# Kernel optimization log

Measured on AMD Instinct MI355X. Metric: run time of the kernel, lower is better.

The kernel has to match this reference:

```python
import jax, jax.numpy as jnp
import numpy as np

H = 1152; NH = 16; HD = 72; INTER = 4304; DEPTH = 4
C = 3; T = 2; P = 16; G = 48; M = 2; S = G * G
MERGED = H * M * M; OUT = 2048; ROT = HD // 2  # rotary_pos_emb_dim = head_dim//2


def _ln(x, w, b, eps=1e-6):
    # manual LayerNorm decomposition (mean/var/rsqrt), fp32 like the original
    m = x.mean(-1, keepdims=True)
    xc = x - m
    v = (xc * xc).mean(-1, keepdims=True)
    return w * (xc * jax.lax.rsqrt(v + eps)) + b


def _gelu(x):
    return jax.nn.gelu(x, approximate=True)  # tanh approximation


def _rot_half(x):
    h = x.shape[-1] // 2
    return jnp.concatenate([-x[..., h:], x[..., :h]], axis=-1)


def _pos_ids():
    # Qwen merge-pattern token order: 2x2 spatial blocks are contiguous
    ids = np.arange(G * G).reshape(G // M, M, G // M, M).transpose(0, 2, 1, 3).reshape(-1)
    return jnp.asarray(ids, dtype=jnp.int32)


def setup_inputs() -> dict:
    key = jax.random.key(0)
    ks = jax.random.split(key, 16)
    w = lambda k, shape: jax.random.normal(k, shape, jnp.float32) * 0.02
    return {
        'pixel_values': jax.random.normal(ks[0], (S, C * T * P * P), jnp.float32),
        'cu_seqlens': jnp.array([0, S], jnp.int32),
        'conv_w': w(ks[1], (H, C, T, P, P)),
        'conv_b': jnp.zeros((H,), jnp.float32),
        'pos_tab': w(ks[2], (G * G, H)),
        'ln1_w': jnp.ones((DEPTH, H), jnp.float32), 'ln1_b': jnp.zeros((DEPTH, H), jnp.float32),
        'ln2_w': jnp.ones((DEPTH, H), jnp.float32), 'ln2_b': jnp.zeros((DEPTH, H), jnp.float32),
        'qkv_w': w(ks[3], (DEPTH, 3 * H, H)), 'qkv_b': jnp.zeros((DEPTH, 3 * H), jnp.float32),
        'proj_w': w(ks[4], (DEPTH, H, H)), 'proj_b': jnp.zeros((DEPTH, H), jnp.float32),
        'fc1_w': w(ks[5], (DEPTH, INTER, H)), 'fc1_b': jnp.zeros((DEPTH, INTER), jnp.float32),
        'fc2_w': w(ks[6], (DEPTH, H, INTER)), 'fc2_b': jnp.zeros((DEPTH, H), jnp.float32),
        'm_norm_w': jnp.ones((H,), jnp.float32), 'm_norm_b': jnp.zeros((H,), jnp.float32),
        'm_fc1_w': w(ks[7], (MERGED, MERGED)), 'm_fc1_b': jnp.zeros((MERGED,), jnp.float32),
        'm_fc2_w': w(ks[8], (OUT, MERGED)), 'm_fc2_b': jnp.zeros((OUT,), jnp.float32),
    }


def reference(pixel_values, cu_seqlens, conv_w, conv_b, pos_tab,
              ln1_w, ln1_b, ln2_w, ln2_b, qkv_w, qkv_b, proj_w, proj_b,
              fc1_w, fc1_b, fc2_w, fc2_b, m_norm_w, m_norm_b,
              m_fc1_w, m_fc1_b, m_fc2_w, m_fc2_b):
    pos_ids = _pos_ids()
    # Conv3d with stride == kernel over pre-extracted patches == matmul
    x = pixel_values @ conv_w.reshape(H, -1).T + conv_b            # [S, H]
    x = x + pos_tab[pos_ids]
    # 2D rotary: h-freqs and w-freqs each ROT/2 dims, concat -> ROT, dup -> HD
    inv_freq = 1.0 / (10000.0 ** (jnp.arange(0, ROT, 2, dtype=jnp.float32) / ROT))
    hp = (pos_ids // G).astype(jnp.float32)
    wp = (pos_ids % G).astype(jnp.float32)
    freqs = jnp.concatenate([hp[:, None] * inv_freq, wp[:, None] * inv_freq], axis=-1)  # [S, ROT]
    emb = jnp.concatenate([freqs, freqs], axis=-1)                 # [S, HD]
    cos = jnp.cos(emb)[:, None, :]                                 # [S, 1, HD]
    sin = jnp.sin(emb)[:, None, :]
    # varlen attention: block-diagonal mask from cu_seqlens
    seg = jnp.searchsorted(cu_seqlens, jnp.arange(S), side='right')
    mask = jnp.where(seg[:, None] == seg[None, :], 0.0, -1e9).astype(jnp.float32)
    scale = 1.0 / np.sqrt(HD)
    for i in range(DEPTH):
        h = _ln(x, ln1_w[i], ln1_b[i])
        qkv = (h @ qkv_w[i].T + qkv_b[i]).reshape(S, 3, NH, HD)
        q, k, v = qkv[:, 0], qkv[:, 1], qkv[:, 2]
        q = q * cos + _rot_half(q) * sin
        k = k * cos + _rot_half(k) * sin
        scores = jnp.einsum('qhd,khd->hqk', q, k) * scale + mask
        attn = jax.nn.softmax(scores, axis=-1)
        o = jnp.einsum('hqk,khd->qhd', attn, v).reshape(S, H)
        x = x + o @ proj_w[i].T + proj_b[i]
        h2 = _ln(x, ln2_w[i], ln2_b[i])
        x = x + _gelu(h2 @ fc1_w[i].T + fc1_b[i]) @ fc2_w[i].T + fc2_b[i]
    # patch merger: pre-merge LN -> reshape to merged -> fc1 -> gelu(tanh) -> fc2
    y = _ln(x, m_norm_w, m_norm_b).reshape(-1, MERGED)             # [S/4, MERGED]
    return _gelu(y @ m_fc1_w.T + m_fc1_b) @ m_fc2_w.T + m_fc2_b   # [S/4, OUT]
```

## Files before the change

### kernel.cpp

```cpp
#include <hip/hip_runtime.h>
#include <hip/hip_bf16.h>
#include <math.h>

#define S 2304
#define HDIM 1152
#define NHEAD 16
#define HD 72
#define INTER 4304
#define INTERP 4352
#define DEPTH 4
#define MERGED 4608
#define OUTD 2048
#define KIN 1536
#define NSPLIT 2
#define KHALF (S / NSPLIT)

typedef float f4 __attribute__((ext_vector_type(4)));
typedef short s8v __attribute__((ext_vector_type(8)));

__device__ __forceinline__ int pos_id_of(int s) {
  int a = s / 96;
  int r = s % 96;
  int b = r >> 2;
  int c = (r >> 1) & 1;
  int d = r & 1;
  return a * 96 + c * 48 + b * 2 + d;
}

__device__ __forceinline__ float gelu_f(float v) {
  const float c = 0.7978845608028654f;
  float t = tanhf(c * (v + 0.044715f * v * v * v));
  return 0.5f * v * (1.f + t);
}

__device__ __forceinline__ unsigned short f2b(float f) {
  unsigned int u = __float_as_uint(f);
  u += 0x7fffu + ((u >> 16) & 1u);
  return (unsigned short)(u >> 16);
}
__device__ __forceinline__ float b2f(unsigned short u) {
  return __uint_as_float(((unsigned int)u) << 16);
}

__device__ __forceinline__ void gload16(const void* g, void* l) {
  __builtin_amdgcn_global_load_lds(
      (const __attribute__((address_space(1))) void*)g,
      (__attribute__((address_space(3))) void*)l, 16, 0, 0);
}

__device__ __forceinline__ int xcd_swz(int flat, int nwg) {
  int q = nwg >> 3, r8 = nwg & 7;
  int xcd = flat & 7, lin = flat >> 3;
  return (xcd < r8 ? xcd * (q + 1) : r8 * (q + 1) + (xcd - r8) * q) + lin;
}

__global__ void __launch_bounds__(256) cvt_kernel(
    const float* __restrict__ src, unsigned short* __restrict__ dst,
    int N, int Ksrc, int Kdst)
{
  int idx = blockIdx.x * 256 + threadIdx.x;
  int kc = Kdst >> 3;
  if (idx >= N * kc) return;
  int r = idx / kc;
  int c8 = (idx % kc) << 3;
  const float* sp = src + (size_t)r * Ksrc + c8;
  unsigned short outv[8];
#pragma unroll
  for (int e = 0; e < 8; ++e)
    outv[e] = (c8 + e < Ksrc) ? f2b(sp[e]) : (unsigned short)0;
  *(uint4*)(dst + (size_t)r * Kdst + c8) = *(uint4*)outv;
}

__global__ void __launch_bounds__(256) gemm_bf16_kernel(
    const unsigned short* __restrict__ A, const unsigned short* __restrict__ B,
    const float* __restrict__ bias, const float* __restrict__ resid,
    void* __restrict__ Cout, int M, int Nreal, int K,
    int lda, int ldb, int ldc, int act, int outbf)
{
  __shared__ unsigned short Asm[2][128 * 32];
  __shared__ unsigned short Bsm[2][128 * 32];
  const int tid = threadIdx.x;
  const int lane = tid & 63;
  const int wv = tid >> 6;
  const int wr = wv >> 1, wc = wv & 1;

  int flat = blockIdx.y * gridDim.x + blockIdx.x;
  int swz = xcd_swz(flat, gridDim.x * gridDim.y);
  const int bm = (swz / gridDim.x) * 128;
  const int bn = (swz % gridDim.x) * 128;

  const int g8 = (lane >> 4) << 3;
  const int lr = lane & 15;

  const int srow = wv * 32 + (lane >> 2);
  const int kcol = (lane & 3) << 3;
  int ar0 = bm + srow;      if (ar0 >= M) ar0 = M - 1;
  int ar1 = bm + srow + 16; if (ar1 >= M) ar1 = M - 1;
  int br0 = bn + srow;      if (br0 >= Nreal) br0 = Nreal - 1;
  int br1 = bn + srow + 16; if (br1 >= Nreal) br1 = Nreal - 1;
  const unsigned short* Ag0 = A + (size_t)ar0 * lda + kcol;
  const unsigned short* Ag1 = A + (size_t)ar1 * lda + kcol;
  const unsigned short* Bg0 = B + (size_t)br0 * ldb + kcol;
  const unsigned short* Bg1 = B + (size_t)br1 * ldb + kcol;

  f4 acc[4][4];
#pragma unroll
  for (int m = 0; m < 4; ++m)
#pragma unroll
    for (int n = 0; n < 4; ++n) { acc[m][n].x = 0.f; acc[m][n].y = 0.f; acc[m][n].z = 0.f; acc[m][n].w = 0.f; }

  const int nt = K >> 5;
  gload16(Ag0, &Asm[0][(wv * 32) * 32]);
  gload16(Ag1, &Asm[0][(wv * 32 + 16) * 32]);
  gload16(Bg0, &Bsm[0][(wv * 32) * 32]);
  gload16(Bg1, &Bsm[0][(wv * 32 + 16) * 32]);
  asm volatile("s_waitcnt vmcnt(0)" ::: "memory");
  __syncthreads();

  int cur = 0;
  for (int t = 0; t < nt; ++t) {
    if (t + 1 < nt) {
      int ko = (t + 1) << 5;
      gload16(Ag0 + ko, &Asm[cur ^ 1][(wv * 32) * 32]);
      gload16(Ag1 + ko, &Asm[cur ^ 1][(wv * 32 + 16) * 32]);
      gload16(Bg0 + ko, &Bsm[cur ^ 1][(wv * 32) * 32]);
      gload16(Bg1 + ko, &Bsm[cur ^ 1][(wv * 32 + 16) * 32]);
    }
    s8v af[4], bf[4];
#pragma unroll
    for (int m = 0; m < 4; ++m)
      af[m] = *(const s8v*)&Asm[cur][(wr * 64 + m * 16 + lr) * 32 + g8];
#pragma unroll
    for (int n = 0; n < 4; ++n)
      bf[n] = *(const s8v*)&Bsm[cur][(wc * 64 + n * 16 + lr) * 32 + g8];
#pragma unroll
    for (int m = 0; m < 4; ++m)
#pragma unroll
      for (int n = 0; n < 4; ++n)
        acc[m][n] = __builtin_amdgcn_mfma_f32_16x16x32_bf16(af[m], bf[n], acc[m][n], 0, 0, 0);
    asm volatile("s_waitcnt vmcnt(0)" ::: "memory");
    __syncthreads();
    cur ^= 1;
  }

  const int g4 = (lane >> 4) << 2;
#pragma unroll
  for (int m = 0; m < 4; ++m) {
    int r = bm + wr * 64 + m * 16 + g4;
#pragma unroll
    for (int n = 0; n < 4; ++n) {
      int cidx = bn + wc * 64 + n * 16 + lr;
      float bb = (cidx < Nreal) ? bias[cidx] : 0.f;
#pragma unroll
      for (int j = 0; j < 4; ++j) {
        int rr = r + j;
        if (rr < M) {
          float v = acc[m][n][j] + bb;
          if (act) v = gelu_f(v);
          if (cidx >= Nreal) v = 0.f;
          if (resid) v += resid[(size_t)rr * ldc + cidx];
          if (outbf) ((unsigned short*)Cout)[(size_t)rr * ldc + cidx] = f2b(v);
          else       ((float*)Cout)[(size_t)rr * ldc + cidx] = v;
        }
      }
    }
  }
}

__global__ void __launch_bounds__(256) gemm_bf16_splitk_kernel(
    const unsigned short* __restrict__ A, const unsigned short* __restrict__ B,
    float* __restrict__ Cpart, int M, int N, int Kc, int lda, int ldb)
{
  __shared__ unsigned short Asm[2][128 * 32];
  __shared__ unsigned short Bsm[2][128 * 32];
  const int tid = threadIdx.x;
  const int lane = tid & 63;
  const int wv = tid >> 6;
  const int wr = wv >> 1, wc = wv & 1;

  int flat = blockIdx.y * gridDim.x + blockIdx.x;
  int swz = xcd_swz(flat, gridDim.x * gridDim.y);
  const int bm = (swz / gridDim.x) * 128;
  const int bn = (swz % gridDim.x) * 128;
  const int z = blockIdx.z;
  const int kbase = z * Kc;

  const int g8 = (lane >> 4) << 3;
  const int lr = lane & 15;

  const int srow = wv * 32 + (lane >> 2);
  const int kcol = (lane & 3) << 3;
  int ar0 = bm + srow;      if (ar0 >= M) ar0 = M - 1;
  int ar1 = bm + srow + 16; if (ar1 >= M) ar1 = M - 1;
  int br0 = bn + srow;      if (br0 >= N) br0 = N - 1;
  int br1 = bn + srow + 16; if (br1 >= N) br1 = N - 1;
  const unsigned short* Ag0 = A + (size_t)ar0 * lda + kbase + kcol;
  const unsigned short* Ag1 = A + (size_t)ar1 * lda + kbase + kcol;
  const unsigned short* Bg0 = B + (size_t)br0 * ldb + kbase + kcol;
  const unsigned short* Bg1 = B + (size_t)br1 * ldb + kbase + kcol;

  f4 acc[4][4];
#pragma unroll
  for (int m = 0; m < 4; ++m)
#pragma unroll
    for (int n = 0; n < 4; ++n) { acc[m][n].x = 0.f; acc[m][n].y = 0.f; acc[m][n].z = 0.f; acc[m][n].w = 0.f; }

  const int nt = Kc >> 5;
  gload16(Ag0, &Asm[0][(wv * 32) * 32]);
  gload16(Ag1, &Asm[0][(wv * 32 + 16) * 32]);
  gload16(Bg0, &Bsm[0][(wv * 32) * 32]);
  gload16(Bg1, &Bsm[0][(wv * 32 + 16) * 32]);
  asm volatile("s_waitcnt vmcnt(0)" ::: "memory");
  __syncthreads();

  int cur = 0;
  for (int t = 0; t < nt; ++t) {
    if (t + 1 < nt) {
      int ko = (t + 1) << 5;
      gload16(Ag0 + ko, &Asm[cur ^ 1][(wv * 32) * 32]);
      gload16(Ag1 + ko, &Asm[cur ^ 1][(wv * 32 + 16) * 32]);
      gload16(Bg0 + ko, &Bsm[cur ^ 1][(wv * 32) * 32]);
      gload16(Bg1 + ko, &Bsm[cur ^ 1][(wv * 32 + 16) * 32]);
    }
    s8v af[4], bf[4];
#pragma unroll
    for (int m = 0; m < 4; ++m)
      af[m] = *(const s8v*)&Asm[cur][(wr * 64 + m * 16 + lr) * 32 + g8];
#pragma unroll
    for (int n = 0; n < 4; ++n)
      bf[n] = *(const s8v*)&Bsm[cur][(wc * 64 + n * 16 + lr) * 32 + g8];
#pragma unroll
    for (int m = 0; m < 4; ++m)
#pragma unroll
      for (int n = 0; n < 4; ++n)
        acc[m][n] = __builtin_amdgcn_mfma_f32_16x16x32_bf16(af[m], bf[n], acc[m][n], 0, 0, 0);
    asm volatile("s_waitcnt vmcnt(0)" ::: "memory");
    __syncthreads();
    cur ^= 1;
  }

  float* Cz = Cpart + (size_t)z * M * N;
  const int g4 = (lane >> 4) << 2;
#pragma unroll
  for (int m = 0; m < 4; ++m) {
    int r = bm + wr * 64 + m * 16 + g4;
#pragma unroll
    for (int n = 0; n < 4; ++n) {
      int cidx = bn + wc * 64 + n * 16 + lr;
      if (cidx < N) {
#pragma unroll
        for (int j = 0; j < 4; ++j) {
          int rr = r + j;
          if (rr < M) Cz[(size_t)rr * N + cidx] = acc[m][n][j];
        }
      }
    }
  }
}

__global__ void __launch_bounds__(256) combine_gemm_kernel(
    const float* __restrict__ Cpart, int nz, const float* __restrict__ bias,
    const float* __restrict__ resid, float* __restrict__ out, int M, int N)
{
  int idx = blockIdx.x * 256 + threadIdx.x;
  int total = (M * N) >> 2;
  if (idx >= total) return;
  int r = idx / (N >> 2);
  int c4 = (idx % (N >> 2)) << 2;
  size_t off = (size_t)r * N + c4;
  float4 s = *(const float4*)(Cpart + off);
  for (int z = 1; z < nz; ++z) {
    float4 p = *(const float4*)(Cpart + (size_t)z * M * N + off);
    s.x += p.x; s.y += p.y; s.z += p.z; s.w += p.w;
  }
  float4 b = *(const float4*)(bias + c4);
  s.x += b.x; s.y += b.y; s.z += b.z; s.w += b.w;
  if (resid) {
    float4 rv = *(const float4*)(resid + off);
    s.x += rv.x; s.y += rv.y; s.z += rv.z; s.w += rv.w;
  }
  *(float4*)(out + off) = s;
}

__global__ void __launch_bounds__(256) ln_kernel(const float* __restrict__ xin,
    const float* __restrict__ w, const float* __restrict__ b, unsigned short* __restrict__ out)
{
  __shared__ float red[8];
  const int row = blockIdx.x;
  const float* xr = xin + (size_t)row * HDIM;
  float s = 0.f;
  for (int i = threadIdx.x; i < HDIM; i += 256) s += xr[i];
#pragma unroll
  for (int off = 32; off > 0; off >>= 1) s += __shfl_down(s, off);
  if ((threadIdx.x & 63) == 0) red[threadIdx.x >> 6] = s;
  __syncthreads();
  float mean = (red[0] + red[1] + red[2] + red[3]) * (1.f / HDIM);
  float s2 = 0.f;
  for (int i = threadIdx.x; i < HDIM; i += 256) { float d = xr[i] - mean; s2 += d * d; }
#pragma unroll
  for (int off = 32; off > 0; off >>= 1) s2 += __shfl_down(s2, off);
  __syncthreads();
  if ((threadIdx.x & 63) == 0) red[threadIdx.x >> 6] = s2;
  __syncthreads();
  float var = (red[0] + red[1] + red[2] + red[3]) * (1.f / HDIM);
  float rstd = rsqrtf(var + 1e-6f);
  for (int i = threadIdx.x; i < HDIM; i += 256)
    out[(size_t)row * HDIM + i] = f2b(w[i] * ((xr[i] - mean) * rstd) + b[i]);
}

__global__ void __launch_bounds__(256) add_pos_kernel(float* __restrict__ x, const float* __restrict__ pos_tab)
{
  int s = blockIdx.x;
  int pid = pos_id_of(s);
  const float* pr = pos_tab + (size_t)pid * HDIM;
  float* xr = x + (size_t)s * HDIM;
  for (int i = threadIdx.x; i < HDIM; i += 256) xr[i] += pr[i];
}

__global__ void rope_tables_kernel(float* __restrict__ cosT, float* __restrict__ sinT)
{
  int s = blockIdx.x;
  int j = threadIdx.x;
  if (j >= 36) return;
  int pid = pos_id_of(s);
  float hp = (float)(pid / 48);
  float wp = (float)(pid % 48);
  int f = (j < 18) ? j : (j - 18);
  float inv = powf(10000.f, -(2.f * (float)f) / 36.f);
  float ang = ((j < 18) ? hp : wp) * inv;
  cosT[s * 36 + j] = cosf(ang);
  sinT[s * 36 + j] = sinf(ang);
}

__global__ void seg_kernel(const int* __restrict__ cu, int n_cu, int* __restrict__ seg)
{
  int i = blockIdx.x * 256 + threadIdx.x;
  if (i >= S) return;
  int s = 0;
  for (int t = 0; t < n_cu; ++t) s += (cu[t] <= i) ? 1 : 0;
  seg[i] = s;
}

__global__ void __launch_bounds__(256) rope_kernel(unsigned short* __restrict__ qkv,
    const float* __restrict__ cosT, const float* __restrict__ sinT)
{
  int idx = blockIdx.x * 256 + threadIdx.x;
  int d = idx % 36; int t = idx / 36;
  int hh = t % NHEAD; t /= NHEAD;
  int qk = t & 1; int s = t >> 1;
  unsigned short* base = qkv + (size_t)s * 3456 + qk * 1152 + hh * 72;
  float c = cosT[s * 36 + d], sn = sinT[s * 36 + d];
  float x0 = b2f(base[d]), x1 = b2f(base[d + 36]);
  base[d] = f2b(x0 * c - x1 * sn);
  base[d + 36] = f2b(x1 * c + x0 * sn);
}

#define KT 64
#define KSL 88
#define ASCALE 0.11785113019775793f

__global__ void __launch_bounds__(256) flash_mfma_kernel(
    const unsigned short* __restrict__ qkv, unsigned short* __restrict__ opart,
    float* __restrict__ ml, const int* __restrict__ seg)
{
  __shared__ __align__(16) unsigned short Ks[64 * KSL];
  __shared__ __align__(16) unsigned short Vt[80 * 72];
  __shared__ __align__(16) unsigned short Ps[4][16 * 72];

  const int tid = threadIdx.x;
  const int lane = tid & 63;
  const int wv = tid >> 6;
  const int g = lane >> 4;
  const int c = lane & 15;

  int flat = (blockIdx.z * NHEAD + blockIdx.y) * (S / 64) + blockIdx.x;
  int swz = xcd_swz(flat, (S / 64) * NHEAD * NSPLIT);
  const int q0 = (swz % (S / 64)) * 64;
  const int hh = (swz / (S / 64)) % NHEAD;
  const int sidx = swz / ((S / 64) * NHEAD);
  const int kbeg = sidx * KHALF;

  for (int i = tid; i < 64 * 8; i += 256) {
    int r = i >> 3, cc = i & 7;
    *(unsigned int*)&Ks[r * KSL + 72 + cc * 2] = 0u;
  }
  for (int i = tid; i < 288; i += 256)
    *(unsigned int*)&Vt[72 * 72 + i * 2] = 0u;

  s8v qf[3];
  {
    const int qrow = q0 + wv * 16 + c;
    const unsigned short* qb = qkv + (size_t)qrow * 3456 + hh * HD;
#pragma unroll
    for (int ks = 0; ks < 3; ++ks) {
      int k = ks * 32 + g * 8;
      if (k <= 64) qf[ks] = *(const s8v*)(qb + k);
      else {
        s8v z;
#pragma unroll
        for (int t = 0; t < 8; ++t) z[t] = 0;
        qf[ks] = z;
      }
    }
  }

  int msg[4];
#pragma unroll
  for (int j = 0; j < 4; ++j) msg[j] = seg[q0 + wv * 16 + g * 4 + j];

  float mj[4], lj[4];
#pragma unroll
  for (int j = 0; j < 4; ++j) { mj[j] = -1e30f; lj[j] = 0.f; }
  f4 acco[5];
#pragma unroll
  for (int n = 0; n < 5; ++n) { acco[n].x = 0.f; acco[n].y = 0.f; acco[n].z = 0.f; acco[n].w = 0.f; }

  uint4 kreg[3], vreg[3];

#define STAGE_LOAD(KT0)                                                                  \
  {                                                                                      \
    _Pragma("unroll")                                                                    \
    for (int ii = 0; ii < 3; ++ii) {                                                     \
      int idx = tid + ii * 256;                                                          \
      if (idx < 576) {                                                                   \
        int rK = idx / 9, cK = idx % 9;                                                  \
        kreg[ii] = *(const uint4*)(qkv + (size_t)((KT0) + rK) * 3456 + 1152 + hh * HD + cK * 8); \
        int rV = idx & 63, cV = idx >> 6;                                                \
        vreg[ii] = *(const uint4*)(qkv + (size_t)((KT0) + rV) * 3456 + 2304 + hh * HD + cV * 8); \
      }                                                                                  \
    }                                                                                    \
  }

#define STAGE_WRITE()                                                                    \
  {                                                                                      \
    _Pragma("unroll")                                                                    \
    for (int ii = 0; ii < 3; ++ii) {                                                     \
      int idx = tid + ii * 256;                                                          \
      if (idx < 576) {                                                                   \
        int rK = idx / 9, cK = idx % 9;                                                  \
        *(uint4*)&Ks[rK * KSL + cK * 8] = kreg[ii];                                      \
        int rV = idx & 63, cV = idx >> 6;                                                \
        unsigned short vv[8];                                                            \
        *(uint4*)vv = vreg[ii];                                                          \
        _Pragma("unroll")                                                                \
        for (int e = 0; e < 8; ++e) Vt[(cV * 8 + e) * 72 + rV] = vv[e];                  \
      }                                                                                  \
    }                                                                                    \
  }

  STAGE_LOAD(kbeg);
  asm volatile("s_waitcnt vmcnt(0)" ::: "memory");
  STAGE_WRITE();
  asm volatile("s_waitcnt lgkmcnt(0)" ::: "memory");
  __builtin_amdgcn_s_barrier();
  __builtin_amdgcn_sched_barrier(0);

  for (int k0 = kbeg; k0 < kbeg + KHALF; k0 += KT) {
    const bool more = (k0 + KT < kbeg + KHALF);
    if (more) STAGE_LOAD(k0 + KT);

    int sgn[4];
#pragma unroll
    for (int n = 0; n < 4; ++n) sgn[n] = seg[k0 + n * 16 + c];

    f4 accs[4];
#pragma unroll
    for (int n = 0; n < 4; ++n) { accs[n].x = 0.f; accs[n].y = 0.f; accs[n].z = 0.f; accs[n].w = 0.f; }
#pragma unroll
    for (int ks = 0; ks < 3; ++ks) {
      const int koff = (ks < 2) ? (ks * 32 + g * 8) : 64;
#pragma unroll
      for (int n = 0; n < 4; ++n) {
        s8v bk = *(const s8v*)&Ks[(n * 16 + c) * KSL + koff];
        accs[n] = __builtin_amdgcn_mfma_f32_16x16x32_bf16(qf[ks], bk, accs[n], 0, 0, 0);
      }
    }

    float sc[4][4], mx[4];
#pragma unroll
    for (int j = 0; j < 4; ++j) mx[j] = -1e30f;
#pragma unroll
    for (int n = 0; n < 4; ++n)
#pragma unroll
      for (int j = 0; j < 4; ++j) {
        float v = accs[n][j] * ASCALE + ((sgn[n] == msg[j]) ? 0.f : -1e9f);
        sc[n][j] = v;
        mx[j] = fmaxf(mx[j], v);
      }
#pragma unroll
    for (int j = 0; j < 4; ++j) {
      mx[j] = fmaxf(mx[j], __shfl_xor(mx[j], 1));
      mx[j] = fmaxf(mx[j], __shfl_xor(mx[j], 2));
      mx[j] = fmaxf(mx[j], __shfl_xor(mx[j], 4));
      mx[j] = fmaxf(mx[j], __shfl_xor(mx[j], 8));
    }
    float alpha[4], rs[4];
#pragma unroll
    for (int j = 0; j < 4; ++j) {
      float mn = fmaxf(mj[j], mx[j]);
      alpha[j] = __expf(mj[j] - mn);
      mj[j] = mn;
      rs[j] = 0.f;
    }
    float pv[4][4];
#pragma unroll
    for (int n = 0; n < 4; ++n)
#pragma unroll
      for (int j = 0; j < 4; ++j) {
        float p = __expf(sc[n][j] - mj[j]);
        pv[n][j] = p;
        rs[j] += p;
      }
#pragma unroll
    for (int j = 0; j < 4; ++j) {
      rs[j] += __shfl_xor(rs[j], 1);
      rs[j] += __shfl_xor(rs[j], 2);
      rs[j] += __shfl_xor(rs[j], 4);
      rs[j] += __shfl_xor(rs[j], 8);
      lj[j] = lj[j] * alpha[j] + rs[j];
    }
#pragma unroll
    for (int n = 0; n < 4; ++n)
#pragma unroll
      for (int j = 0; j < 4; ++j)
        Ps[wv][(g * 4 + j) * 72 + n * 16 + c] = f2b(pv[n][j]);

#pragma unroll
    for (int n = 0; n < 5; ++n)
#pragma unroll
      for (int j = 0; j < 4; ++j) acco[n][j] *= alpha[j];

    asm volatile("s_waitcnt lgkmcnt(0)" ::: "memory");
    __builtin_amdgcn_sched_barrier(0);

#pragma unroll
    for (int ks = 0; ks < 2; ++ks) {
      s8v pa = *(const s8v*)&Ps[wv][c * 72 + ks * 32 + g * 8];
#pragma unroll
      for (int n = 0; n < 5; ++n) {
        s8v vb = *(const s8v*)&Vt[(n * 16 + c) * 72 + ks * 32 + g * 8];
        acco[n] = __builtin_amdgcn_mfma_f32_16x16x32_bf16(pa, vb, acco[n], 0, 0, 0);
      }
    }

    asm volatile("s_waitcnt lgkmcnt(0)" ::: "memory");
    __builtin_amdgcn_s_barrier();
    if (more) {
      asm volatile("s_waitcnt vmcnt(0)" ::: "memory");
      STAGE_WRITE();
      asm volatile("s_waitcnt lgkmcnt(0)" ::: "memory");
    }
    __builtin_amdgcn_s_barrier();
    __builtin_amdgcn_sched_barrier(0);
  }

  unsigned short* op = opart + (size_t)(sidx * NHEAD + hh) * S * 72;
#pragma unroll
  for (int n = 0; n < 5; ++n) {
    int col = n * 16 + c;
    if (col < HD) {
#pragma unroll
      for (int j = 0; j < 4; ++j) {
        int row = q0 + wv * 16 + g * 4 + j;
        op[(size_t)row * 72 + col] = f2b(acco[n][j]);
      }
    }
  }
  if (c == 0) {
#pragma unroll
    for (int j = 0; j < 4; ++j) {
      int row = q0 + wv * 16 + g * 4 + j;
      float2 v; v.x = mj[j]; v.y = lj[j];
      *(float2*)&ml[((size_t)(sidx * NHEAD + hh) * S + row) * 2] = v;
    }
  }
}

__global__ void __launch_bounds__(256) attn_combine_kernel(
    const unsigned short* __restrict__ opart, const float* __restrict__ ml,
    unsigned short* __restrict__ oout)
{
  int idx = blockIdx.x * 256 + threadIdx.x;
  int d = idx % 72;
  int row = (idx / 72) % S;
  int hh = idx / (72 * S);
  size_t b1 = (size_t)hh * S + row;
  size_t b2 = (size_t)(NHEAD + hh) * S + row;
  float m1 = ml[b1 * 2], l1 = ml[b1 * 2 + 1];
  float m2 = ml[b2 * 2], l2 = ml[b2 * 2 + 1];
  float ms = fmaxf(m1, m2);
  float a1 = __expf(m1 - ms), a2 = __expf(m2 - ms);
  float l = a1 * l1 + a2 * l2;
  float o = (a1 * b2f(opart[b1 * 72 + d]) + a2 * b2f(opart[b2 * 72 + d])) / l;
  oout[(size_t)row * HDIM + hh * 72 + d] = f2b(o);
}

extern "C" void kernel_launch(void* const* d_in, const int* in_sizes, int n_in,
                              void* d_out, int out_size, void* d_ws, size_t ws_size,
                              hipStream_t stream)
{
  (void)n_in; (void)out_size; (void)ws_size;
  const float* pix    = (const float*)d_in[0];
  const int*   cu     = (const int*)d_in[1];
  const int    n_cu   = in_sizes[1];
  const float* conv_w = (const float*)d_in[2];
  const float* conv_b = (const float*)d_in[3];
  const float* pos_tab= (const float*)d_in[4];
  const float* ln1_w  = (const float*)d_in[5];
  const float* ln1_b  = (const float*)d_in[6];
  const float* ln2_w  = (const float*)d_in[7];
  const float* ln2_b  = (const float*)d_in[8];
  const float* qkv_w  = (const float*)d_in[9];
  const float* qkv_b  = (const float*)d_in[10];
  const float* proj_w = (const float*)d_in[11];
  const float* proj_b = (const float*)d_in[12];
  const float* fc1_w  = (const float*)d_in[13];
  const float* fc1_b  = (const float*)d_in[14];
  const float* fc2_w  = (const float*)d_in[15];
  const float* fc2_b  = (const float*)d_in[16];
  const float* mn_w   = (const float*)d_in[17];
  const float* mn_b   = (const float*)d_in[18];
  const float* mf1_w  = (const float*)d_in[19];
  const float* mf1_b  = (const float*)d_in[20];
  const float* mf2_w  = (const float*)d_in[21];
  const float* mf2_b  = (const float*)d_in[22];
  float* out = (float*)d_out;

  float*    x      = (float*)d_ws;
  unsigned short* h_bf   = (unsigned short*)(x + (size_t)S * HDIM);
  unsigned short* qkv_bf = h_bf + (size_t)S * HDIM;
  unsigned short* A_bf   = qkv_bf + (size_t)S * 3456;
  unsigned short* Wbuf   = A_bf + (size_t)S * INTERP;
  float*    cosT   = (float*)(Wbuf + (size_t)MERGED * MERGED);
  float*    sinT   = cosT + (size_t)S * 36;
  int*      seg    = (int*)(sinT + (size_t)S * 36);
  unsigned short* pix_bf = A_bf;
  unsigned short* opart  = A_bf;
  float*    ml     = (float*)(A_bf + (size_t)NSPLIT * NHEAD * S * 72);
  float*    part_h = (float*)h_bf;
  float*    part_q = (float*)qkv_bf;

  auto cvt = [&](const float* src, unsigned short* dst, int N, int Ksrc, int Kdst) {
    int total = N * (Kdst >> 3);
    cvt_kernel<<<(total + 255) / 256, 256, 0, stream>>>(src, dst, N, Ksrc, Kdst);
  };
  auto gemm = [&](const unsigned short* A, const unsigned short* B, const float* bias,
                  const float* resid, void* C, int M, int N, int K,
                  int lda, int ldb, int ldc, int act, int outbf) {
    gemm_bf16_kernel<<<dim3((N + 127) / 128, (M + 127) / 128), 256, 0, stream>>>(
        A, B, bias, resid, C, M, N, K, lda, ldb, ldc, act, outbf);
  };
  auto gemm_sk = [&](const unsigned short* A, const unsigned short* B, float* part,
                     const float* bias, const float* resid, float* C,
                     int M, int N, int K, int nz, int lda, int ldb) {
    gemm_bf16_splitk_kernel<<<dim3(N / 128, (M + 127) / 128, nz), 256, 0, stream>>>(
        A, B, part, M, N, K / nz, lda, ldb);
    combine_gemm_kernel<<<((M * N / 4) + 255) / 256, 256, 0, stream>>>(
        part, nz, bias, resid, C, M, N);
  };

  cvt(pix, pix_bf, S, KIN, KIN);
  cvt(conv_w, Wbuf, HDIM, KIN, KIN);
  gemm_sk(pix_bf, Wbuf, part_h, conv_b, nullptr, x, S, HDIM, KIN, 2, KIN, KIN);
  add_pos_kernel<<<S, 256, 0, stream>>>(x, pos_tab);
  rope_tables_kernel<<<S, 64, 0, stream>>>(cosT, sinT);
  seg_kernel<<<(S + 255) / 256, 256, 0, stream>>>(cu, n_cu, seg);

  for (int layer = 0; layer < DEPTH; ++layer) {
    ln_kernel<<<S, 256, 0, stream>>>(x, ln1_w + layer * HDIM, ln1_b + layer * HDIM, h_bf);
    cvt(qkv_w + (size_t)layer * 3456 * HDIM, Wbuf, 3456, HDIM, HDIM);
    gemm(h_bf, Wbuf, qkv_b + layer * 3456, nullptr, qkv_bf, S, 3456, HDIM, HDIM, HDIM, 3456, 0, 1);
    rope_kernel<<<(S * 2 * NHEAD * 36) / 256, 256, 0, stream>>>(qkv_bf, cosT, sinT);
    flash_mfma_kernel<<<dim3(S / 64, NHEAD, NSPLIT), 256, 0, stream>>>(qkv_bf, opart, ml, seg);
    attn_combine_kernel<<<(NHEAD * S * 72) / 256, 256, 0, stream>>>(opart, ml, h_bf);
    cvt(proj_w + (size_t)layer * HDIM * HDIM, Wbuf, HDIM, HDIM, HDIM);
    gemm_sk(h_bf, Wbuf, part_q, proj_b + layer * HDIM, x, x, S, HDIM, HDIM, 3, HDIM, HDIM);
    ln_kernel<<<S, 256, 0, stream>>>(x, ln2_w + layer * HDIM, ln2_b + layer * HDIM, h_bf);
    cvt(fc1_w + (size_t)layer * INTER * HDIM, Wbuf, INTER, HDIM, HDIM);
    gemm(h_bf, Wbuf, fc1_b + layer * INTER, nullptr, A_bf, S, INTER, HDIM, HDIM, HDIM, INTERP, 1, 1);
    cvt(fc2_w + (size_t)layer * HDIM * INTER, Wbuf, HDIM, INTER, INTERP);
    gemm_sk(A_bf, Wbuf, part_h, fc2_b + layer * HDIM, x, x, S, HDIM, INTERP, 2, INTERP, INTERP);
  }

  ln_kernel<<<S, 256, 0, stream>>>(x, mn_w, mn_b, h_bf);
  cvt(mf1_w, Wbuf, MERGED, MERGED, MERGED);
  gemm(h_bf, Wbuf, mf1_b, nullptr, A_bf, 576, MERGED, MERGED, MERGED, MERGED, MERGED, 1, 1);
  cvt(mf2_w, Wbuf, OUTD, MERGED, MERGED);
  gemm_sk(A_bf, Wbuf, part_h, mf2_b, nullptr, out, 576, OUTD, MERGED, 4, MERGED, MERGED);
}
```

Before: 1.879 ms.

## Add 64-row GEMM tile kernel and restructure flash attention softmax layout

Adds a new GEMM kernel with 64x128 tiles, used for the QKV, fc1 and merger fc1 projections, so more blocks are launched and the GPU's compute units are better filled. Separately, the flash attention kernel swaps the MFMA operand order so that each lane owns one query row. This lets row max and sum reductions use two cross-lane shuffles instead of four per row. It also adds a fast path that skips the segment mask when the whole tile lies in one segment. The smaller GEMM tile lowers data reuse per block, and the attention change adds extra shuffles to broadcast rescale factors.

```diff
diff --git a/kernel.cpp b/kernel.cpp
--- a/kernel.cpp
+++ b/kernel.cpp
@@ -167,6 +167,92 @@
   }
 }
 
+__global__ void __launch_bounds__(256) gemm_bf16_m64_kernel(
+    const unsigned short* __restrict__ A, const unsigned short* __restrict__ B,
+    const float* __restrict__ bias, void* __restrict__ Cout,
+    int M, int Nreal, int K, int lda, int ldb, int ldc, int act, int outbf)
+{
+  __shared__ unsigned short Asm[2][64 * 32];
+  __shared__ unsigned short Bsm[2][128 * 32];
+  const int tid = threadIdx.x;
+  const int lane = tid & 63;
+  const int wv = tid >> 6;
+
+  int flat = blockIdx.y * gridDim.x + blockIdx.x;
+  int swz = xcd_swz(flat, gridDim.x * gridDim.y);
+  const int bm = (swz / gridDim.x) * 64;
+  const int bn = (swz % gridDim.x) * 128;
+
+  const int g8 = (lane >> 4) << 3;
+  const int lr = lane & 15;
+
+  const int lrow = lane >> 2;
+  const int kq = (lane & 3) << 3;
+  const unsigned short* AgP = A + (size_t)(bm + wv * 16 + lrow) * lda + kq;
+  int brow1 = bn + wv * 16 + lrow;      if (brow1 >= Nreal) brow1 = Nreal - 1;
+  int brow2 = bn + 64 + wv * 16 + lrow; if (brow2 >= Nreal) brow2 = Nreal - 1;
+  const unsigned short* BgP1 = B + (size_t)brow1 * ldb + kq;
+  const unsigned short* BgP2 = B + (size_t)brow2 * ldb + kq;
+
+  f4 acc[4][2];
+#pragma unroll
+  for (int m = 0; m < 4; ++m)
+#pragma unroll
+    for (int n = 0; n < 2; ++n) { acc[m][n].x = 0.f; acc[m][n].y = 0.f; acc[m][n].z = 0.f; acc[m][n].w = 0.f; }
+
+  const int nt = K >> 5;
+  gload16(AgP, &Asm[0][(wv * 16) * 32]);
+  gload16(BgP1, &Bsm[0][(wv * 16) * 32]);
+  gload16(BgP2, &Bsm[0][(64 + wv * 16) * 32]);
+  asm volatile("s_waitcnt vmcnt(0)" ::: "memory");
+  __syncthreads();
+
+  int cur = 0;
+  for (int t = 0; t < nt; ++t) {
+    if (t + 1 < nt) {
+      int ko = (t + 1) << 5;
+      gload16(AgP + ko, &Asm[cur ^ 1][(wv * 16) * 32]);
+      gload16(BgP1 + ko, &Bsm[cur ^ 1][(wv * 16) * 32]);
+      gload16(BgP2 + ko, &Bsm[cur ^ 1][(64 + wv * 16) * 32]);
+    }
+    s8v af[4], bf[2];
+#pragma unroll
+    for (int m = 0; m < 4; ++m)
+      af[m] = *(const s8v*)&Asm[cur][(m * 16 + lr) * 32 + g8];
+#pragma unroll
+    for (int n = 0; n < 2; ++n)
+      bf[n] = *(const s8v*)&Bsm[cur][(wv * 32 + n * 16 + lr) * 32 + g8];
+#pragma unroll
+    for (int m = 0; m < 4; ++m)
+#pragma unroll
+      for (int n = 0; n < 2; ++n)
+        acc[m][n] = __builtin_amdgcn_mfma_f32_16x16x32_bf16(af[m], bf[n], acc[m][n], 0, 0, 0);
+    asm volatile("s_waitcnt vmcnt(0)" ::: "memory");
+    __syncthreads();
+    cur ^= 1;
+  }
+
+  const int g4 = (lane >> 4) << 2;
+#pragma unroll
+  for (int m = 0; m < 4; ++m) {
+    int r = bm + m * 16 + g4;
+#pragma unroll
+    for (int n = 0; n < 2; ++n) {
+      int cidx = bn + wv * 32 + n * 16 + lr;
+      float bb = (cidx < Nreal) ? bias[cidx] : 0.f;
+#pragma unroll
+      for (int j = 0; j < 4; ++j) {
+        int rr = r + j;
+        float v = acc[m][n][j] + bb;
+        if (act) v = gelu_f(v);
+        if (cidx >= Nreal) v = 0.f;
+        if (outbf) ((unsigned short*)Cout)[(size_t)rr * ldc + cidx] = f2b(v);
+        else       ((float*)Cout)[(size_t)rr * ldc + cidx] = v;
+      }
+    }
+  }
+}
+
 __global__ void __launch_bounds__(256) gemm_bf16_splitk_kernel(
     const unsigned short* __restrict__ A, const unsigned short* __restrict__ B,
     float* __restrict__ Cpart, int M, int N, int Kc, int lda, int ldb)
@@ -387,6 +473,10 @@
   for (int i = tid; i < 288; i += 256)
     *(unsigned int*)&Vt[72 * 72 + i * 2] = 0u;
 
+  const bool uni = (seg[q0] == seg[q0 + 63]) && (seg[kbeg] == seg[kbeg + KHALF - 1])
+                && (seg[q0] == seg[kbeg]);
+  const int msgc = seg[q0 + wv * 16 + c];
+
   s8v qf[3];
   {
     const int qrow = q0 + wv * 16 + c;
@@ -404,13 +494,7 @@
     }
   }
 
-  int msg[4];
-#pragma unroll
-  for (int j = 0; j < 4; ++j) msg[j] = seg[q0 + wv * 16 + g * 4 + j];
-
-  float mj[4], lj[4];
-#pragma unroll
-  for (int j = 0; j < 4; ++j) { mj[j] = -1e30f; lj[j] = 0.f; }
+  float m_c = -1e30f, l_c = 0.f;
   f4 acco[5];
 #pragma unroll
   for (int n = 0; n < 5; ++n) { acco[n].x = 0.f; acco[n].y = 0.f; acco[n].z = 0.f; acco[n].w = 0.f; }
@@ -459,76 +543,76 @@
     const bool more = (k0 + KT < kbeg + KHALF);
     if (more) STAGE_LOAD(k0 + KT);
 
-    int sgn[4];
-#pragma unroll
-    for (int n = 0; n < 4; ++n) sgn[n] = seg[k0 + n * 16 + c];
-
     f4 accs[4];
 #pragma unroll
-    for (int n = 0; n < 4; ++n) { accs[n].x = 0.f; accs[n].y = 0.f; accs[n].z = 0.f; accs[n].w = 0.f; }
+    for (int nk = 0; nk < 4; ++nk) { accs[nk].x = 0.f; accs[nk].y = 0.f; accs[nk].z = 0.f; accs[nk].w = 0.f; }
 #pragma unroll
     for (int ks = 0; ks < 3; ++ks) {
       const int koff = (ks < 2) ? (ks * 32 + g * 8) : 64;
 #pragma unroll
-      for (int n = 0; n < 4; ++n) {
-        s8v bk = *(const s8v*)&Ks[(n * 16 + c) * KSL + koff];
-        accs[n] = __builtin_amdgcn_mfma_f32_16x16x32_bf16(qf[ks], bk, accs[n], 0, 0, 0);
+      for (int nk = 0; nk < 4; ++nk) {
+        s8v bk = *(const s8v*)&Ks[(nk * 16 + c) * KSL + koff];
+        accs[nk] = __builtin_amdgcn_mfma_f32_16x16x32_bf16(bk, qf[ks], accs[nk], 0, 0, 0);
       }
     }
 
-    float sc[4][4], mx[4];
-#pragma unroll
-    for (int j = 0; j < 4; ++j) mx[j] = -1e30f;
-#pragma unroll
-    for (int n = 0; n < 4; ++n)
+    float sc[4][4];
+    float mx = -1e30f;
+    if (uni) {
+#pragma unroll
+      for (int nk = 0; nk < 4; ++nk)
+#pragma unroll
+        for (int j = 0; j < 4; ++j) {
+          float v = accs[nk][j] * ASCALE;
+          sc[nk][j] = v;
+          mx = fmaxf(mx, v);
+        }
+    } else {
+#pragma unroll
+      for (int nk = 0; nk < 4; ++nk)
+#pragma unroll
+        for (int j = 0; j < 4; ++j) {
+          int kk = k0 + nk * 16 + g * 4 + j;
+          float v = accs[nk][j] * ASCALE + ((seg[kk] == msgc) ? 0.f : -1e9f);
+          sc[nk][j] = v;
+          mx = fmaxf(mx, v);
+        }
+    }
+    mx = fmaxf(mx, __shfl_xor(mx, 16));
+    mx = fmaxf(mx, __shfl_xor(mx, 32));
+    float mn = fmaxf(m_c, mx);
+    float alpha_c = __expf(m_c - mn);
+    m_c = mn;
+    float rsum = 0.f;
+    float p[4][4];
+#pragma unroll
+    for (int nk = 0; nk < 4; ++nk)
 #pragma unroll
       for (int j = 0; j < 4; ++j) {
-        float v = accs[n][j] * ASCALE + ((sgn[n] == msg[j]) ? 0.f : -1e9f);
-        sc[n][j] = v;
-        mx[j] = fmaxf(mx[j], v);
+        float pv = __expf(sc[nk][j] - mn);
+        p[nk][j] = pv;
+        rsum += pv;
       }
-#pragma unroll
-    for (int j = 0; j < 4; ++j) {
-      mx[j] = fmaxf(mx[j], __shfl_xor(mx[j], 1));
-      mx[j] = fmaxf(mx[j], __shfl_xor(mx[j], 2));
-      mx[j] = fmaxf(mx[j], __shfl_xor(mx[j], 4));
-      mx[j] = fmaxf(mx[j], __shfl_xor(mx[j], 8));
-    }
-    float alpha[4], rs[4];
-#pragma unroll
-    for (int j = 0; j < 4; ++j) {
-      float mn = fmaxf(mj[j], mx[j]);
-      alpha[j] = __expf(mj[j] - mn);
-      mj[j] = mn;
-      rs[j] = 0.f;
-    }
-    float pv[4][4];
-#pragma unroll
-    for (int n = 0; n < 4; ++n)
-#pragma unroll
-      for (int j = 0; j < 4; ++j) {
-        float p = __expf(sc[n][j] - mj[j]);
-        pv[n][j] = p;
-        rs[j] += p;
-      }
-#pragma unroll
-    for (int j = 0; j < 4; ++j) {
-      rs[j] += __shfl_xor(rs[j], 1);
-      rs[j] += __shfl_xor(rs[j], 2);
-      rs[j] += __shfl_xor(rs[j], 4);
-      rs[j] += __shfl_xor(rs[j], 8);
-      lj[j] = lj[j] * alpha[j] + rs[j];
-    }
-#pragma unroll
-    for (int n = 0; n < 4; ++n)
-#pragma unroll
-      for (int j = 0; j < 4; ++j)
-        Ps[wv][(g * 4 + j) * 72 + n * 16 + c] = f2b(pv[n][j]);
-
+    rsum += __shfl_xor(rsum, 16);
+    rsum += __shfl_xor(rsum, 32);
+    l_c = l_c * alpha_c + rsum;
+
+#pragma unroll
+    for (int nk = 0; nk < 4; ++nk) {
+      unsigned int w0 = (unsigned int)f2b(p[nk][0]) | ((unsigned int)f2b(p[nk][1]) << 16);
+      unsigned int w1 = (unsigned int)f2b(p[nk][2]) | ((unsigned int)f2b(p[nk][3]) << 16);
+      uint2 wv2; wv2.x = w0; wv2.y = w1;
+      *(uint2*)&Ps[wv][c * 72 + nk * 16 + g * 4] = wv2;
+    }
+
+    float alpha_row[4];
+#pragma unroll
+    for (int j = 0; j < 4; ++j)
+      alpha_row[j] = __shfl(alpha_c, (lane & 48) | (g * 4 + j));
 #pragma unroll
     for (int n = 0; n < 5; ++n)
 #pragma unroll
-      for (int j = 0; j < 4; ++j) acco[n][j] *= alpha[j];
+      for (int j = 0; j < 4; ++j) acco[n][j] *= alpha_row[j];
 
     asm volatile("s_waitcnt lgkmcnt(0)" ::: "memory");
     __builtin_amdgcn_sched_barrier(0);
@@ -554,6 +638,13 @@
     __builtin_amdgcn_sched_barrier(0);
   }
 
+  float l_row[4], m_row[4];
+#pragma unroll
+  for (int j = 0; j < 4; ++j) {
+    l_row[j] = __shfl(l_c, (lane & 48) | (g * 4 + j));
+    m_row[j] = __shfl(m_c, (lane & 48) | (g * 4 + j));
+  }
+
   unsigned short* op = opart + (size_t)(sidx * NHEAD + hh) * S * 72;
 #pragma unroll
   for (int n = 0; n < 5; ++n) {
@@ -570,7 +661,7 @@
 #pragma unroll
     for (int j = 0; j < 4; ++j) {
       int row = q0 + wv * 16 + g * 4 + j;
-      float2 v; v.x = mj[j]; v.y = lj[j];
+      float2 v; v.x = m_row[j]; v.y = l_row[j];
       *(float2*)&ml[((size_t)(sidx * NHEAD + hh) * S + row) * 2] = v;
     }
   }
@@ -650,6 +741,11 @@
     gemm_bf16_kernel<<<dim3((N + 127) / 128, (M + 127) / 128), 256, 0, stream>>>(
         A, B, bias, resid, C, M, N, K, lda, ldb, ldc, act, outbf);
   };
+  auto gemm64 = [&](const unsigned short* A, const unsigned short* B, const float* bias,
+                    void* C, int M, int N, int K, int lda, int ldb, int ldc, int act, int outbf) {
+    gemm_bf16_m64_kernel<<<dim3((N + 127) / 128, M / 64), 256, 0, stream>>>(
+        A, B, bias, C, M, N, K, lda, ldb, ldc, act, outbf);
+  };
   auto gemm_sk = [&](const unsigned short* A, const unsigned short* B, float* part,
                      const float* bias, const float* resid, float* C,
                      int M, int N, int K, int nz, int lda, int ldb) {
@@ -669,7 +765,7 @@
   for (int layer = 0; layer < DEPTH; ++layer) {
     ln_kernel<<<S, 256, 0, stream>>>(x, ln1_w + layer * HDIM, ln1_b + layer * HDIM, h_bf);
     cvt(qkv_w + (size_t)layer * 3456 * HDIM, Wbuf, 3456, HDIM, HDIM);
-    gemm(h_bf, Wbuf, qkv_b + layer * 3456, nullptr, qkv_bf, S, 3456, HDIM, HDIM, HDIM, 3456, 0, 1);
+    gemm64(h_bf, Wbuf, qkv_b + layer * 3456, qkv_bf, S, 3456, HDIM, HDIM, HDIM, 3456, 0, 1);
     rope_kernel<<<(S * 2 * NHEAD * 36) / 256, 256, 0, stream>>>(qkv_bf, cosT, sinT);
     flash_mfma_kernel<<<dim3(S / 64, NHEAD, NSPLIT), 256, 0, stream>>>(qkv_bf, opart, ml, seg);
     attn_combine_kernel<<<(NHEAD * S * 72) / 256, 256, 0, stream>>>(opart, ml, h_bf);
@@ -677,14 +773,14 @@
     gemm_sk(h_bf, Wbuf, part_q, proj_b + layer * HDIM, x, x, S, HDIM, HDIM, 3, HDIM, HDIM);
     ln_kernel<<<S, 256, 0, stream>>>(x, ln2_w + layer * HDIM, ln2_b + layer * HDIM, h_bf);
     cvt(fc1_w + (size_t)layer * INTER * HDIM, Wbuf, INTER, HDIM, HDIM);
-    gemm(h_bf, Wbuf, fc1_b + layer * INTER, nullptr, A_bf, S, INTER, HDIM, HDIM, HDIM, INTERP, 1, 1);
+    gemm64(h_bf, Wbuf, fc1_b + layer * INTER, A_bf, S, INTER, HDIM, HDIM, HDIM, INTERP, 1, 1);
     cvt(fc2_w + (size_t)layer * HDIM * INTER, Wbuf, HDIM, INTER, INTERP);
     gemm_sk(A_bf, Wbuf, part_h, fc2_b + layer * HDIM, x, x, S, HDIM, INTERP, 2, INTERP, INTERP);
   }
 
   ln_kernel<<<S, 256, 0, stream>>>(x, mn_w, mn_b, h_bf);
   cvt(mf1_w, Wbuf, MERGED, MERGED, MERGED);
-  gemm(h_bf, Wbuf, mf1_b, nullptr, A_bf, 576, MERGED, MERGED, MERGED, MERGED, MERGED, 1, 1);
+  gemm64(h_bf, Wbuf, mf1_b, A_bf, 576, MERGED, MERGED, MERGED, MERGED, MERGED, 1, 1);
   cvt(mf2_w, Wbuf, OUTD, MERGED, MERGED);
   gemm_sk(A_bf, Wbuf, part_h, mf2_b, nullptr, out, 576, OUTD, MERGED, 4, MERGED, MERGED);
 }
```

Measured after the change: 1.796 ms. 1.05x faster.
